# Optimization experiments

Measured on AMD Instinct MI355X. Metric: run time of the kernel, lower is better.

The kernel has to match this reference:

```python
import jax, jax.numpy as jnp
import numpy as np

RADIUS = 5            # min(max(5, ceil(80/20)), 80) = 5
SPATIAL_SIGMA = 4.0
INTENSITY_SIGMA = 1.0
EPS_MEAN = 1e-5
EPS_DEN = 1e-6


def gaussian_kernel(radius, sigma, dtype):
    # norm.pdf(d/sigma)/norm.pdf(0) == exp(-d^2 / (2*sigma^2))
    x2 = jnp.arange(-radius, radius + 1, dtype=dtype) ** 2
    d2 = x2[:, None, None] + x2[None, :, None] + x2[None, None, :]
    k = jnp.exp(-d2 / (2.0 * sigma * sigma))
    return k[None, None]  # OIDHW: [1,1,2r+1,2r+1,2r+1]


def conv3d_same(x, kernel):
    # x: [B,1,H,W,D]; 'same' padding with radius on all spatial dims
    pad = [(RADIUS, RADIUS)] * 3
    return jax.lax.conv_general_dilated(
        x, kernel, window_strides=(1, 1, 1), padding=pad,
        dimension_numbers=('NCDHW', 'OIDHW', 'NCDHW'))


def setup_inputs() -> dict:
    key = jax.random.key(0)
    k1, k2 = jax.random.split(key)
    labels = jax.random.uniform(k1, (2, 4, 80, 80, 80), dtype=jnp.float32)
    inputs = jax.random.uniform(k2, (2, 1, 80, 80, 80), dtype=jnp.float32)
    return {"labels": labels, "inputs": inputs}


def reference(labels, inputs):
    N, K, H, W, D = labels.shape
    kernel = gaussian_kernel(RADIUS, SPATIAL_SIGMA, labels.dtype)

    probs = labels[:, :, None]          # [N,K,1,H,W,D]
    img = inputs[:, None]               # [N,1,C,H,W,D]

    # per-class mean intensity: [N,K,C,1,1,1]
    class_mean = (jnp.mean(img * probs, axis=(3, 4, 5), keepdims=True)
                  / (jnp.mean(probs, axis=(3, 4, 5), keepdims=True) + EPS_MEAN))
    diff = jnp.sum((img - class_mean) ** 2, axis=2)        # [N,K,H,W,D]
    weights = jnp.exp(-(diff ** 2) / (INTENSITY_SIGMA ** 2))  # [N,K,H,W,D]

    # batch the K independent single-channel 3D convs as [N*K,1,H,W,D]
    pw = (labels * weights).reshape(N * K, 1, H, W, D)
    w = weights.reshape(N * K, 1, H, W, D)
    conv_pw = conv3d_same(pw, kernel).reshape(N, K, H, W, D)
    conv_w = conv3d_same(w, kernel).reshape(N, K, H, W, D)

    numerator = jnp.sum(labels * conv_pw, axis=(2, 3, 4))   # [N,K]
    denominator = jnp.sum(labels * conv_w, axis=(2, 3, 4))  # [N,K]
    ratio = numerator / (denominator + EPS_DEN)

    # torch L1Loss(num/den, 0) = mean over batch N, summed over classes k
    loss = jnp.sum(jnp.mean(jnp.abs(ratio), axis=0))
    return K - loss
```

## Files before the change

kernel.cpp:

```cpp
#include <hip/hip_runtime.h>
#include <math.h>

#define RAD 5
#define SIDE 80
#define SLAB 6400
#define VOL 512000
#define NCH 8
#define NCLS 4
#define TW 16
#define NT 5
#define CPART (SIDE*NT)
#define NBLK (NCH*SIDE*NT)
#define Q 20
#define TAS 24
#define TBS 21

__constant__ float GW[11] = {
    0.45783336177161427f, 0.6065306597126334f, 0.7548396019890073f,
    0.8824969025845955f,  0.969233234476344f,  1.0f,
    0.969233234476344f,   0.8824969025845955f, 0.7548396019890073f,
    0.6065306597126334f,  0.45783336177161427f};

__device__ float  g_bufT[(size_t)NCH * VOL];
__device__ float2 g_part1[NBLK];
__device__ float2 g_part2[NBLK];

__global__ void __launch_bounds__(256) convdw_sums_kernel(
        const float* __restrict__ labels, const float* __restrict__ img) {
    const int blk = blockIdx.x;
    const int c   = blk / (SIDE * NT);
    const int rem = blk % (SIDE * NT);
    const int h   = rem / NT;
    const int w0  = (rem % NT) * TW;
    const int n   = c >> 2;

    __shared__ float4 tA[26 * TAS];
    __shared__ float4 tB[26 * TBS];
    __shared__ float sm[8];

    for (int i = threadIdx.x; i < 26 * 4; i += 256) {
        int r = i >> 2, j = i & 3;
        tA[r * TAS + ((j < 2) ? j : (20 + j))] = make_float4(0.f, 0.f, 0.f, 0.f);
    }
    const float* labc = labels + ((size_t)c * SIDE + h) * SLAB;
    for (int i = threadIdx.x; i < 26 * Q; i += 256) {
        int r = i / Q, q = i - r * Q;
        int w = w0 - RAD + r;
        float4 v = (w >= 0 && w < SIDE)
                     ? ((const float4*)(labc + (size_t)w * SIDE))[q]
                     : make_float4(0.f, 0.f, 0.f, 0.f);
        tA[r * TAS + 2 + q] = v;
    }
    __syncthreads();

    float sip = 0.f, sp = 0.f;
    const float4* imgc4 = (const float4*)(img + ((((size_t)n * SIDE + h) * SIDE + w0) * SIDE));
    for (int i = threadIdx.x; i < TW * Q; i += 256) {
        int rl = i / Q, q = i - rl * Q;
        float4 l = tA[(rl + RAD) * TAS + 2 + q];
        float4 v = imgc4[i];
        sip += l.x * v.x + l.y * v.y + l.z * v.z + l.w * v.w;
        sp  += l.x + l.y + l.z + l.w;
    }

    for (int i = threadIdx.x; i < 26 * Q; i += 256) {
        int r = i / Q, q = i - r * Q;
        const float4* row = &tA[r * TAS + q];
        float a[20];
        #pragma unroll
        for (int j = 0; j < 5; ++j) {
            float4 v = row[j];
            a[4 * j] = v.x; a[4 * j + 1] = v.y; a[4 * j + 2] = v.z; a[4 * j + 3] = v.w;
        }
        float4 o;
        float s0 = 0.f, s1 = 0.f, s2 = 0.f, s3 = 0.f;
        #pragma unroll
        for (int t = 0; t < 11; ++t) {
            float g = GW[t];
            s0 += g * a[t + 3]; s1 += g * a[t + 4];
            s2 += g * a[t + 5]; s3 += g * a[t + 6];
        }
        o.x = s0; o.y = s1; o.z = s2; o.w = s3;
        tB[r * TBS + q] = o;
    }

    #pragma unroll
    for (int off = 32; off > 0; off >>= 1) {
        sip += __shfl_down(sip, off);
        sp  += __shfl_down(sp, off);
    }
    const int lane = threadIdx.x & 63;
    const int wid  = threadIdx.x >> 6;
    if (lane == 0) { sm[wid * 2] = sip; sm[wid * 2 + 1] = sp; }
    __syncthreads();
    if (threadIdx.x == 0)
        g_part1[blk] = make_float2(sm[0] + sm[2] + sm[4] + sm[6],
                                   sm[1] + sm[3] + sm[5] + sm[7]);

    float* outc = g_bufT + (size_t)c * VOL + (size_t)h * SIDE;
    for (int i = threadIdx.x; i < TW * Q; i += 256) {
        int rl = i / Q, q = i - rl * Q;
        float sx = 0.f, sy = 0.f, sz = 0.f, sw = 0.f;
        #pragma unroll
        for (int t = 0; t < 11; ++t) {
            float g = GW[t];
            float4 v = tB[(rl + t) * TBS + q];
            sx += g * v.x; sy += g * v.y; sz += g * v.z; sw += g * v.w;
        }
        ((float4*)(outc + (size_t)(w0 + rl) * SLAB))[q] = make_float4(sx, sy, sz, sw);
    }
}

__global__ void __launch_bounds__(256) convh_dot_kernel(
        const float* __restrict__ labels, const float* __restrict__ img) {
    const int blk = blockIdx.x;
    const int c   = blk / (SIDE * NT);
    const int rem = blk % (SIDE * NT);
    const int w   = rem / NT;
    const int h0  = (rem % NT) * TW;
    const int n   = c >> 2;

    __shared__ float4 tile[26 * TBS];
    __shared__ float sm[8];
    __shared__ float s_mean;

    float a = 0.f, b = 0.f;
    for (int t = threadIdx.x; t < CPART; t += 256) {
        float2 p = g_part1[c * CPART + t];
        a += p.x; b += p.y;
    }
    #pragma unroll
    for (int off = 32; off > 0; off >>= 1) {
        a += __shfl_down(a, off);
        b += __shfl_down(b, off);
    }
    const int lane = threadIdx.x & 63;
    const int wid  = threadIdx.x >> 6;
    if (lane == 0) { sm[wid * 2] = a; sm[wid * 2 + 1] = b; }

    const float4* bc4 = (const float4*)(g_bufT + (size_t)c * VOL + (size_t)w * SLAB);
    for (int i = threadIdx.x; i < 26 * Q; i += 256) {
        int r = i / Q, q = i - r * Q;
        int hh = h0 - RAD + r;
        float4 v = (hh >= 0 && hh < SIDE) ? bc4[hh * Q + q]
                                          : make_float4(0.f, 0.f, 0.f, 0.f);
        tile[r * TBS + q] = v;
    }
    __syncthreads();
    if (threadIdx.x == 0)
        s_mean = (sm[0] + sm[2] + sm[4] + sm[6]) /
                 (sm[1] + sm[3] + sm[5] + sm[7] + 5.12f);
    __syncthreads();
    const float mean = s_mean;

    const float4* labp4 = (const float4*)(labels + (size_t)c * VOL);
    const float4* imgp4 = (const float4*)(img + (size_t)n * VOL);
    float num = 0.f, den = 0.f;
    for (int i = threadIdx.x; i < TW * Q; i += 256) {
        int hl = i / Q, q = i - hl * Q;
        float sx = 0.f, sy = 0.f, sz = 0.f, sw = 0.f;
        #pragma unroll
        for (int t = 0; t < 11; ++t) {
            float g = GW[t];
            float4 v = tile[(hl + t) * TBS + q];
            sx += g * v.x; sy += g * v.y; sz += g * v.z; sw += g * v.w;
        }
        size_t gi = ((size_t)(h0 + hl) * SIDE + w) * Q + q;
        float4 l = labp4[gi];
        float4 v = imgp4[gi];
        float d0 = v.x - mean, d1 = v.y - mean, d2 = v.z - mean, d3 = v.w - mean;
        float q0 = d0 * d0, q1 = d1 * d1, q2 = d2 * d2, q3 = d3 * d3;
        float w0_ = __expf(-q0 * q0), w1_ = __expf(-q1 * q1);
        float w2_ = __expf(-q2 * q2), w3_ = __expf(-q3 * q3);
        num += sx * l.x * w0_ + sy * l.y * w1_ + sz * l.z * w2_ + sw * l.w * w3_;
        den += sx * w0_ + sy * w1_ + sz * w2_ + sw * w3_;
    }
    #pragma unroll
    for (int off = 32; off > 0; off >>= 1) {
        num += __shfl_down(num, off);
        den += __shfl_down(den, off);
    }
    if (lane == 0) { sm[wid * 2] = num; sm[wid * 2 + 1] = den; }
    __syncthreads();
    if (threadIdx.x == 0)
        g_part2[blk] = make_float2(sm[0] + sm[2] + sm[4] + sm[6],
                                   sm[1] + sm[3] + sm[5] + sm[7]);
}

__global__ void __launch_bounds__(256) final_kernel(float* __restrict__ out) {
    __shared__ float sm[8];
    __shared__ float cn[NCH], cd[NCH];
    const int lane = threadIdx.x & 63;
    const int wid  = threadIdx.x >> 6;
    for (int c = 0; c < NCH; ++c) {
        float a = 0.f, b = 0.f;
        for (int t = threadIdx.x; t < CPART; t += 256) {
            float2 p = g_part2[c * CPART + t];
            a += p.x; b += p.y;
        }
        #pragma unroll
        for (int off = 32; off > 0; off >>= 1) {
            a += __shfl_down(a, off);
            b += __shfl_down(b, off);
        }
        if (lane == 0) { sm[wid * 2] = a; sm[wid * 2 + 1] = b; }
        __syncthreads();
        if (threadIdx.x == 0) {
            cn[c] = sm[0] + sm[2] + sm[4] + sm[6];
            cd[c] = sm[1] + sm[3] + sm[5] + sm[7];
        }
        __syncthreads();
    }
    if (threadIdx.x == 0) {
        float loss = 0.f;
        for (int k = 0; k < NCLS; ++k) {
            float r0 = cn[k]        / (cd[k]        + 1e-6f);
            float r1 = cn[NCLS + k] / (cd[NCLS + k] + 1e-6f);
            loss += 0.5f * (fabsf(r0) + fabsf(r1));
        }
        out[0] = (float)NCLS - loss;
    }
}

extern "C" void kernel_launch(void* const* d_in, const int* in_sizes, int n_in,
                              void* d_out, int out_size, void* d_ws, size_t ws_size,
                              hipStream_t stream) {
    const float* labels = (const float*)d_in[0];
    const float* img    = (const float*)d_in[1];
    float* out = (float*)d_out;
    (void)d_ws; (void)ws_size;

    hipLaunchKernelGGL(convdw_sums_kernel, dim3(NBLK), dim3(256), 0, stream, labels, img);
    hipLaunchKernelGGL(convh_dot_kernel,   dim3(NBLK), dim3(256), 0, stream, labels, img);
    hipLaunchKernelGGL(final_kernel,       dim3(1),    dim3(256), 0, stream, out);
}
```

Before: 102.9 us.

## Use register sliding windows for h-conv and drop labels shared tile

The first kernel no longer stages labels in a shared tile. Each thread loads its neighbouring float4s straight from global memory and computes the D-direction conv and the partial sums in registers. The second kernel is remapped so each thread owns one (w,q) column and 4 consecutive h outputs, loading a 14-deep register window from the buffer instead of a shared tile. This cuts shared-memory traffic and syncs, and the grid shrinks to 1000 blocks. The cost is redundant global loads (5x per row in the first kernel, 14/4 per output in the second) and higher register pressure.

```diff
diff --git a/kernel.cpp b/kernel.cpp
--- a/kernel.cpp
+++ b/kernel.cpp
@@ -9,11 +9,11 @@
 #define NCLS 4
 #define TW 16
 #define NT 5
-#define CPART (SIDE*NT)
-#define NBLK (NCH*SIDE*NT)
+#define NBLK1 (NCH*SIDE*NT)
 #define Q 20
-#define TAS 24
-#define TBS 21
+#define TBS 22
+#define NBLK2 1000
+#define CPB 125
 
 __constant__ float GW[11] = {
     0.45783336177161427f, 0.6065306597126334f, 0.7548396019890073f,
@@ -22,57 +22,48 @@
     0.6065306597126334f,  0.45783336177161427f};
 
 __device__ float  g_bufT[(size_t)NCH * VOL];
-__device__ float2 g_part1[NBLK];
-__device__ float2 g_part2[NBLK];
+__device__ float2 g_part1[NBLK1];
+__device__ float2 g_part2[NBLK2];
 
 __global__ void __launch_bounds__(256) convdw_sums_kernel(
         const float* __restrict__ labels, const float* __restrict__ img) {
-    const int blk = blockIdx.x;
-    const int c   = blk / (SIDE * NT);
-    const int rem = blk % (SIDE * NT);
+    const int tile = blockIdx.x;
+    const int c   = tile / (SIDE * NT);
+    const int rem = tile % (SIDE * NT);
     const int h   = rem / NT;
     const int w0  = (rem % NT) * TW;
     const int n   = c >> 2;
 
-    __shared__ float4 tA[26 * TAS];
     __shared__ float4 tB[26 * TBS];
     __shared__ float sm[8];
 
-    for (int i = threadIdx.x; i < 26 * 4; i += 256) {
-        int r = i >> 2, j = i & 3;
-        tA[r * TAS + ((j < 2) ? j : (20 + j))] = make_float4(0.f, 0.f, 0.f, 0.f);
-    }
-    const float* labc = labels + ((size_t)c * SIDE + h) * SLAB;
+    const float4* labc4 = (const float4*)(labels + ((size_t)c * SIDE + h) * SLAB);
+    const float4* imgc4 = (const float4*)(img + ((size_t)n * SIDE + h) * SLAB);
+
+    float sip = 0.f, sp = 0.f;
     for (int i = threadIdx.x; i < 26 * Q; i += 256) {
-        int r = i / Q, q = i - r * Q;
-        int w = w0 - RAD + r;
-        float4 v = (w >= 0 && w < SIDE)
-                     ? ((const float4*)(labc + (size_t)w * SIDE))[q]
-                     : make_float4(0.f, 0.f, 0.f, 0.f);
-        tA[r * TAS + 2 + q] = v;
-    }
-    __syncthreads();
-
-    float sip = 0.f, sp = 0.f;
-    const float4* imgc4 = (const float4*)(img + ((((size_t)n * SIDE + h) * SIDE + w0) * SIDE));
-    for (int i = threadIdx.x; i < TW * Q; i += 256) {
-        int rl = i / Q, q = i - rl * Q;
-        float4 l = tA[(rl + RAD) * TAS + 2 + q];
-        float4 v = imgc4[i];
-        sip += l.x * v.x + l.y * v.y + l.z * v.z + l.w * v.w;
-        sp  += l.x + l.y + l.z + l.w;
-    }
-
-    for (int i = threadIdx.x; i < 26 * Q; i += 256) {
-        int r = i / Q, q = i - r * Q;
-        const float4* row = &tA[r * TAS + q];
+        const int r = i / Q, q = i - (i / Q) * Q;
+        const int w = w0 - RAD + r;
         float a[20];
         #pragma unroll
-        for (int j = 0; j < 5; ++j) {
-            float4 v = row[j];
-            a[4 * j] = v.x; a[4 * j + 1] = v.y; a[4 * j + 2] = v.z; a[4 * j + 3] = v.w;
-        }
-        float4 o;
+        for (int j = 0; j < 20; ++j) a[j] = 0.f;
+        if (w >= 0 && w < SIDE) {
+            const float4* row = labc4 + (size_t)w * Q;
+            #pragma unroll
+            for (int j = 0; j < 5; ++j) {
+                int qq = q - 2 + j;
+                if (qq >= 0 && qq < Q) {
+                    float4 v = row[qq];
+                    a[4 * j] = v.x; a[4 * j + 1] = v.y;
+                    a[4 * j + 2] = v.z; a[4 * j + 3] = v.w;
+                }
+            }
+            if (r >= RAD && r < RAD + TW) {
+                float4 v = imgc4[(size_t)w * Q + q];
+                sip += a[8] * v.x + a[9] * v.y + a[10] * v.z + a[11] * v.w;
+                sp  += a[8] + a[9] + a[10] + a[11];
+            }
+        }
         float s0 = 0.f, s1 = 0.f, s2 = 0.f, s3 = 0.f;
         #pragma unroll
         for (int t = 0; t < 11; ++t) {
@@ -80,10 +71,8 @@
             s0 += g * a[t + 3]; s1 += g * a[t + 4];
             s2 += g * a[t + 5]; s3 += g * a[t + 6];
         }
-        o.x = s0; o.y = s1; o.z = s2; o.w = s3;
-        tB[r * TBS + q] = o;
-    }
-
+        tB[r * TBS + q] = make_float4(s0, s1, s2, s3);
+    }
     #pragma unroll
     for (int off = 32; off > 0; off >>= 1) {
         sip += __shfl_down(sip, off);
@@ -94,12 +83,11 @@
     if (lane == 0) { sm[wid * 2] = sip; sm[wid * 2 + 1] = sp; }
     __syncthreads();
     if (threadIdx.x == 0)
-        g_part1[blk] = make_float2(sm[0] + sm[2] + sm[4] + sm[6],
-                                   sm[1] + sm[3] + sm[5] + sm[7]);
-
+        g_part1[tile] = make_float2(sm[0] + sm[2] + sm[4] + sm[6],
+                                    sm[1] + sm[3] + sm[5] + sm[7]);
     float* outc = g_bufT + (size_t)c * VOL + (size_t)h * SIDE;
     for (int i = threadIdx.x; i < TW * Q; i += 256) {
-        int rl = i / Q, q = i - rl * Q;
+        const int rl = i / Q, q = i - (i / Q) * Q;
         float sx = 0.f, sy = 0.f, sz = 0.f, sw = 0.f;
         #pragma unroll
         for (int t = 0; t < 11; ++t) {
@@ -113,20 +101,22 @@
 
 __global__ void __launch_bounds__(256) convh_dot_kernel(
         const float* __restrict__ labels, const float* __restrict__ img) {
-    const int blk = blockIdx.x;
-    const int c   = blk / (SIDE * NT);
-    const int rem = blk % (SIDE * NT);
-    const int w   = rem / NT;
-    const int h0  = (rem % NT) * TW;
+    const int c = blockIdx.x / CPB;
+    const int tid = blockIdx.x * 256 + threadIdx.x;
+    const int rem = tid % (CPB * 256);
+    const int hq  = rem / 1600;
+    const int r2  = rem % 1600;
+    const int w   = r2 / Q;
+    const int q   = r2 % Q;
+    const int h0  = hq * 4;
     const int n   = c >> 2;
 
-    __shared__ float4 tile[26 * TBS];
     __shared__ float sm[8];
     __shared__ float s_mean;
 
     float a = 0.f, b = 0.f;
-    for (int t = threadIdx.x; t < CPART; t += 256) {
-        float2 p = g_part1[c * CPART + t];
+    for (int t = threadIdx.x; t < SIDE * NT; t += 256) {
+        float2 p = g_part1[c * (SIDE * NT) + t];
         a += p.x; b += p.y;
     }
     #pragma unroll
@@ -137,15 +127,6 @@
     const int lane = threadIdx.x & 63;
     const int wid  = threadIdx.x >> 6;
     if (lane == 0) { sm[wid * 2] = a; sm[wid * 2 + 1] = b; }
-
-    const float4* bc4 = (const float4*)(g_bufT + (size_t)c * VOL + (size_t)w * SLAB);
-    for (int i = threadIdx.x; i < 26 * Q; i += 256) {
-        int r = i / Q, q = i - r * Q;
-        int hh = h0 - RAD + r;
-        float4 v = (hh >= 0 && hh < SIDE) ? bc4[hh * Q + q]
-                                          : make_float4(0.f, 0.f, 0.f, 0.f);
-        tile[r * TBS + q] = v;
-    }
     __syncthreads();
     if (threadIdx.x == 0)
         s_mean = (sm[0] + sm[2] + sm[4] + sm[6]) /
@@ -153,19 +134,27 @@
     __syncthreads();
     const float mean = s_mean;
 
-    const float4* labp4 = (const float4*)(labels + (size_t)c * VOL);
-    const float4* imgp4 = (const float4*)(img + (size_t)n * VOL);
+    const float4* bc4 = (const float4*)g_bufT + (size_t)c * (VOL / 4) + (size_t)w * (SLAB / 4);
+    float4 win[14];
+    #pragma unroll
+    for (int m = 0; m < 14; ++m) {
+        int hh = h0 - RAD + m;
+        win[m] = (hh >= 0 && hh < SIDE) ? bc4[hh * Q + q]
+                                        : make_float4(0.f, 0.f, 0.f, 0.f);
+    }
+    const float4* labp4 = (const float4*)labels + (size_t)c * (VOL / 4);
+    const float4* imgp4 = (const float4*)img + (size_t)n * (VOL / 4);
     float num = 0.f, den = 0.f;
-    for (int i = threadIdx.x; i < TW * Q; i += 256) {
-        int hl = i / Q, q = i - hl * Q;
+    #pragma unroll
+    for (int k = 0; k < 4; ++k) {
         float sx = 0.f, sy = 0.f, sz = 0.f, sw = 0.f;
         #pragma unroll
         for (int t = 0; t < 11; ++t) {
             float g = GW[t];
-            float4 v = tile[(hl + t) * TBS + q];
+            float4 v = win[k + t];
             sx += g * v.x; sy += g * v.y; sz += g * v.z; sw += g * v.w;
         }
-        size_t gi = ((size_t)(h0 + hl) * SIDE + w) * Q + q;
+        size_t gi = (size_t)(h0 + k) * (SLAB / 4) + (size_t)w * Q + q;
         float4 l = labp4[gi];
         float4 v = imgp4[gi];
         float d0 = v.x - mean, d1 = v.y - mean, d2 = v.z - mean, d3 = v.w - mean;
@@ -183,8 +172,8 @@
     if (lane == 0) { sm[wid * 2] = num; sm[wid * 2 + 1] = den; }
     __syncthreads();
     if (threadIdx.x == 0)
-        g_part2[blk] = make_float2(sm[0] + sm[2] + sm[4] + sm[6],
-                                   sm[1] + sm[3] + sm[5] + sm[7]);
+        g_part2[blockIdx.x] = make_float2(sm[0] + sm[2] + sm[4] + sm[6],
+                                          sm[1] + sm[3] + sm[5] + sm[7]);
 }
 
 __global__ void __launch_bounds__(256) final_kernel(float* __restrict__ out) {
@@ -194,8 +183,8 @@
     const int wid  = threadIdx.x >> 6;
     for (int c = 0; c < NCH; ++c) {
         float a = 0.f, b = 0.f;
-        for (int t = threadIdx.x; t < CPART; t += 256) {
-            float2 p = g_part2[c * CPART + t];
+        for (int t = threadIdx.x; t < CPB; t += 256) {
+            float2 p = g_part2[c * CPB + t];
             a += p.x; b += p.y;
         }
         #pragma unroll
@@ -230,7 +219,7 @@
     float* out = (float*)d_out;
     (void)d_ws; (void)ws_size;
 
-    hipLaunchKernelGGL(convdw_sums_kernel, dim3(NBLK), dim3(256), 0, stream, labels, img);
-    hipLaunchKernelGGL(convh_dot_kernel,   dim3(NBLK), dim3(256), 0, stream, labels, img);
-    hipLaunchKernelGGL(final_kernel,       dim3(1),    dim3(256), 0, stream, out);
-}
+    hipLaunchKernelGGL(convdw_sums_kernel, dim3(NBLK1), dim3(256), 0, stream, labels, img);
+    hipLaunchKernelGGL(convh_dot_kernel,   dim3(NBLK2), dim3(256), 0, stream, labels, img);
+    hipLaunchKernelGGL(final_kernel,       dim3(1),     dim3(256), 0, stream, out);
+}
```

Result: faster. 98.21 us (-4.5%).
